# Kernel tuning notes

Measured on AMD Instinct MI355X. Metric: run time of the kernel, lower is better.

Reference implementation:

```python
import jax, jax.numpy as jnp
import numpy as np

EPS = 1e-5  # haiku LayerNorm default eps

def _ln(x):
    # LayerNorm over last dim, no scale/offset, use_fast_variance=False
    m = jnp.mean(x, axis=-1, keepdims=True)
    v = jnp.mean((x - m) ** 2, axis=-1, keepdims=True)
    return (x - m) / jnp.sqrt(v + EPS)

def _adaptive_ln(x, cond, gamma_c, Ws, bs, Wb):
    # AdaptiveLayerNorm with single_cond path
    xn = _ln(x)
    cn = _ln(cond) * gamma_c           # single_cond_layer_norm (scale only)
    scale = cn @ Ws + bs               # single_cond_scale (with bias)
    bias = cn @ Wb                     # single_cond_bias (no bias)
    return jax.nn.sigmoid(scale) * xn + bias

def setup_inputs() -> dict:
    key = jax.random.key(0)
    ks = jax.random.split(key, 24)
    B, Q, K, C, H = 2, 3072, 3072, 128, 4
    Dh = C // H
    s = 0.02
    inp = {
        'x_q': jax.random.normal(ks[0], (B, Q, C), jnp.float32),
        'x_k': jax.random.normal(ks[1], (B, K, C), jnp.float32),
        'mask_q': jax.random.randint(ks[2], (B, Q), 0, 2, jnp.int32),
        'mask_k': jax.random.randint(ks[3], (B, K), 0, 2, jnp.int32),
        'pair_logits': jax.random.normal(ks[4], (B, H, Q, K), jnp.float32),
        'single_cond_q': jax.random.normal(ks[5], (B, Q, C), jnp.float32),
        'single_cond_k': jax.random.normal(ks[6], (B, K, C), jnp.float32),
        # AdaptiveLayerNorm q params
        'gamma_cq': jnp.ones((C,), jnp.float32),
        'Wsq': jax.random.normal(ks[7], (C, C), jnp.float32) * s,
        'bsq': jax.random.normal(ks[8], (C,), jnp.float32) * s,
        'Wbq': jax.random.normal(ks[9], (C, C), jnp.float32) * s,
        # AdaptiveLayerNorm k params
        'gamma_ck': jnp.ones((C,), jnp.float32),
        'Wsk': jax.random.normal(ks[10], (C, C), jnp.float32) * s,
        'bsk': jax.random.normal(ks[11], (C,), jnp.float32) * s,
        'Wbk': jax.random.normal(ks[12], (C, C), jnp.float32) * s,
        # attention projections
        'Wq': jax.random.normal(ks[13], (C, H, Dh), jnp.float32) * s,
        'bq': jax.random.normal(ks[14], (1, H, Dh), jnp.float32) * s,
        'Wk': jax.random.normal(ks[15], (C, H, Dh), jnp.float32) * s,
        'Wv': jax.random.normal(ks[16], (C, H, Dh), jnp.float32) * s,
        'Wg': jax.random.normal(ks[17], (C, C), jnp.float32) * s,
        # AdaptiveZeroInit params
        'Wt2': jax.random.normal(ks[18], (C, C), jnp.float32) * s,
        'Wzc': jax.random.normal(ks[19], (C, C), jnp.float32) * s,
        'bzc': jax.random.normal(ks[20], (C,), jnp.float32) * s,
    }
    return inp

def reference(x_q, x_k, mask_q, mask_k, pair_logits, single_cond_q, single_cond_k,
              gamma_cq, Wsq, bsq, Wbq, gamma_ck, Wsk, bsk, Wbk,
              Wq, bq, Wk, Wv, Wg, Wt2, Wzc, bzc):
    mq = mask_q.astype(jnp.float32)
    mk = mask_k.astype(jnp.float32)
    # bias as written in the original: 1e9 * (mq-1)[...,None,:,None] * (mk-1)[...,None,None,:]
    bias = 1e9 * (mq - 1.0)[:, None, :, None] * (mk - 1.0)[:, None, None, :]
    bias = bias + pair_logits  # [B,H,Q,K]

    xq = _adaptive_ln(x_q, single_cond_q, gamma_cq, Wsq, bsq, Wbq)
    xk = _adaptive_ln(x_k, single_cond_k, gamma_ck, Wsk, bsk, Wbk)

    Dh = Wq.shape[-1]
    q = jnp.einsum('bqi,ihd->bqhd', xq, Wq) + bq  # bq [1,H,Dh] broadcasts
    k = jnp.einsum('bki,ihd->bkhd', xk, Wk)
    v = jnp.einsum('bki,ihd->bkhd', xk, Wv)

    logits = jnp.einsum('bqhd,bkhd->bhqk', q * (Dh ** -0.5), k) + bias
    weights = jax.nn.softmax(logits, axis=-1).astype(xq.dtype)
    wa = jnp.einsum('bhqk,bkhd->bqhd', weights, v)
    B, Q, H, _ = wa.shape
    wa = wa.reshape(B, Q, H * Dh)

    wa = wa * jax.nn.sigmoid(xq @ Wg)  # gating_query

    # AdaptiveZeroInit with raw single_cond_q
    out = (wa @ Wt2) * jax.nn.sigmoid(single_cond_q @ Wzc + bzc)
    return out
```

## Files before the change

kernel.cpp:

```cpp
#include <hip/hip_runtime.h>
#include <hip/hip_bf16.h>

typedef unsigned short u16;
typedef unsigned int u32;
typedef __attribute__((ext_vector_type(4))) float f32x4;
typedef __attribute__((ext_vector_type(4))) u32 u32x4;
typedef __attribute__((ext_vector_type(8))) __bf16 bf16x8;

#define SQ 3072
#define NH 4
#define DH 32

static __device__ __forceinline__ u16 f2bf(float f) {
  return __builtin_bit_cast(u16, (__bf16)f);
}
static __device__ __forceinline__ u32 pk2(float a, float b) {
  return (u32)f2bf(a) | ((u32)f2bf(b) << 16);
}
static __device__ __forceinline__ bf16x8 ld8(const u16* p) {
  return __builtin_bit_cast(bf16x8, *reinterpret_cast<const u32x4*>(p));
}
static __device__ __forceinline__ f32x4 mfma16(bf16x8 a, bf16x8 b, f32x4 c) {
  return __builtin_amdgcn_mfma_f32_16x16x32_bf16(a, b, c, 0, 0, 0);
}
static __device__ __forceinline__ float sigm(float x) { return 1.0f / (1.0f + __expf(-x)); }
static __device__ __forceinline__ float red16(float v) {
  v += __shfl_xor(v, 1); v += __shfl_xor(v, 2);
  v += __shfl_xor(v, 4); v += __shfl_xor(v, 8);
  return v;
}

static __device__ __forceinline__ void gemm8(
    const u16* a, const u16* wt, int lr, int lg, int w, f32x4 d[2]) {
  f32x4 z = {0.f, 0.f, 0.f, 0.f};
  d[0] = z; d[1] = z;
#pragma unroll
  for (int kc = 0; kc < 4; ++kc) {
    int ko = kc * 32 + lg * 8;
    bf16x8 a0 = ld8(a + lr * 136 + ko);
    bf16x8 a1 = ld8(a + (16 + lr) * 136 + ko);
    bf16x8 b0 = ld8(wt + (w * 16 + lr) * 128 + ko);
    d[0] = mfma16(a0, b0, d[0]);
    d[1] = mfma16(a1, b0, d[1]);
  }
}

struct PrepSrc { const float* p[10]; };

__global__ __launch_bounds__(256) void prep(PrepSrc s, u16* __restrict__ dst) {
  __shared__ float tl[32][132];
  const int mm = blockIdx.x >> 2, c = blockIdx.x & 3;
  const int tid = threadIdx.x;
  {
    const int krl = tid >> 3, col0 = (tid & 7) * 16;
    const int kr = c * 32 + krl;
    const float* src = s.p[mm] + kr * 128 + col0;
#pragma unroll
    for (int j = 0; j < 4; ++j) {
      f32x4 v = *reinterpret_cast<const f32x4*>(src + j * 4);
      tl[krl][col0 + j * 4 + 0] = v[0];
      tl[krl][col0 + j * 4 + 1] = v[1];
      tl[krl][col0 + j * 4 + 2] = v[2];
      tl[krl][col0 + j * 4 + 3] = v[3];
    }
  }
  __syncthreads();
  const int co = tid >> 1, kc0 = (tid & 1) * 16;
  u32 wbuf[8];
#pragma unroll
  for (int j = 0; j < 8; ++j)
    wbuf[j] = pk2(tl[kc0 + 2 * j][co], tl[kc0 + 2 * j + 1][co]);
  u32x4* dp = reinterpret_cast<u32x4*>(dst + mm * 16384 + co * 128 + c * 32 + kc0);
  u32x4 w0 = {wbuf[0], wbuf[1], wbuf[2], wbuf[3]};
  u32x4 w1 = {wbuf[4], wbuf[5], wbuf[6], wbuf[7]};
  dp[0] = w0; dp[1] = w1;
}

__global__ __launch_bounds__(512) void rowblocks(
    const float* __restrict__ x_q, const float* __restrict__ scq,
    const float* __restrict__ gamma_cq, const float* __restrict__ bsq,
    const float* __restrict__ bq, const float* __restrict__ bzc,
    const float* __restrict__ x_k, const float* __restrict__ sck,
    const float* __restrict__ gamma_ck, const float* __restrict__ bsk,
    const u16* __restrict__ WT,
    u16* __restrict__ qbf, float* __restrict__ gate, float* __restrict__ zc,
    u16* __restrict__ kbf, u16* __restrict__ vT) {
  __shared__ float xnf[32 * 132];
  __shared__ u16 a_cn[32 * 136];
  __shared__ u16 a_raw[32 * 136];
  __shared__ u16 a_xa[32 * 136];
  const int tid = threadIdx.x;
  const bool qside = blockIdx.x < 192;
  const int blk = qside ? blockIdx.x : blockIdx.x - 192;
  const float* x     = qside ? x_q : x_k;
  const float* cond  = qside ? scq : sck;
  const float* gamma = qside ? gamma_cq : gamma_ck;
  const float* bs    = qside ? bsq : bsk;
  const int rl = tid >> 4, sub = tid & 15, c0 = sub * 8;
  const size_t grow = (size_t)blk * 32 + rl;

  {
    float xs[8];
    const float4* xr = reinterpret_cast<const float4*>(x + grow * 128 + c0);
    float4 t0 = xr[0], t1 = xr[1];
    xs[0]=t0.x; xs[1]=t0.y; xs[2]=t0.z; xs[3]=t0.w;
    xs[4]=t1.x; xs[5]=t1.y; xs[6]=t1.z; xs[7]=t1.w;
    float s = 0.f;
#pragma unroll
    for (int i = 0; i < 8; ++i) s += xs[i];
    float mean = red16(s) * (1.f / 128.f);
    float vs = 0.f;
#pragma unroll
    for (int i = 0; i < 8; ++i) { float dd = xs[i] - mean; vs += dd * dd; }
    float rstd = rsqrtf(red16(vs) * (1.f / 128.f) + 1e-5f);
    float4* xw = reinterpret_cast<float4*>(&xnf[rl * 132 + c0]);
    float4 o0, o1;
    o0.x=(xs[0]-mean)*rstd; o0.y=(xs[1]-mean)*rstd; o0.z=(xs[2]-mean)*rstd; o0.w=(xs[3]-mean)*rstd;
    o1.x=(xs[4]-mean)*rstd; o1.y=(xs[5]-mean)*rstd; o1.z=(xs[6]-mean)*rstd; o1.w=(xs[7]-mean)*rstd;
    xw[0] = o0; xw[1] = o1;
  }
  {
    float cs[8], gs[8];
    const float4* cr = reinterpret_cast<const float4*>(cond + grow * 128 + c0);
    const float4* gr = reinterpret_cast<const float4*>(gamma + c0);
    float4 c_0 = cr[0], c_1 = cr[1], g_0 = gr[0], g_1 = gr[1];
    cs[0]=c_0.x; cs[1]=c_0.y; cs[2]=c_0.z; cs[3]=c_0.w;
    cs[4]=c_1.x; cs[5]=c_1.y; cs[6]=c_1.z; cs[7]=c_1.w;
    gs[0]=g_0.x; gs[1]=g_0.y; gs[2]=g_0.z; gs[3]=g_0.w;
    gs[4]=g_1.x; gs[5]=g_1.y; gs[6]=g_1.z; gs[7]=g_1.w;
    float s = 0.f;
#pragma unroll
    for (int i = 0; i < 8; ++i) s += cs[i];
    float mean = red16(s) * (1.f / 128.f);
    float vs = 0.f;
#pragma unroll
    for (int i = 0; i < 8; ++i) { float dd = cs[i] - mean; vs += dd * dd; }
    float rstd = rsqrtf(red16(vs) * (1.f / 128.f) + 1e-5f);
    float cn[8];
#pragma unroll
    for (int i = 0; i < 8; ++i) cn[i] = (cs[i] - mean) * rstd * gs[i];
    u32x4 cw = {pk2(cn[0],cn[1]), pk2(cn[2],cn[3]), pk2(cn[4],cn[5]), pk2(cn[6],cn[7])};
    *reinterpret_cast<u32x4*>(&a_cn[rl * 136 + c0]) = cw;
    if (qside) {
      u32x4 rw = {pk2(cs[0],cs[1]), pk2(cs[2],cs[3]), pk2(cs[4],cs[5]), pk2(cs[6],cs[7])};
      *reinterpret_cast<u32x4*>(&a_raw[rl * 136 + c0]) = rw;
    }
  }
  __syncthreads();
  const int lane = tid & 63, w = tid >> 6, lr = lane & 15, lg = lane >> 4;
  const int wtbase = qside ? 0 : 5;
  f32x4 dS[2], dB[2];
  gemm8(a_cn, WT + (wtbase + 0) * 16384, lr, lg, w, dS);
  gemm8(a_cn, WT + (wtbase + 1) * 16384, lr, lg, w, dB);
  const int col = w * 16 + lr;
#pragma unroll
  for (int mt = 0; mt < 2; ++mt)
#pragma unroll
    for (int r = 0; r < 4; ++r) {
      int rowl = mt * 16 + lg * 4 + r;
      float sc = dS[mt][r] + bs[col];
      float xa = sigm(sc) * xnf[rowl * 132 + col] + dB[mt][r];
      a_xa[rowl * 136 + col] = f2bf(xa);
    }
  __syncthreads();
  if (qside) {
    f32x4 dQ[2], dG[2], dZ[2];
    gemm8(a_xa,  WT + 2 * 16384, lr, lg, w, dQ);
    gemm8(a_xa,  WT + 3 * 16384, lr, lg, w, dG);
    gemm8(a_raw, WT + 4 * 16384, lr, lg, w, dZ);
#pragma unroll
    for (int mt = 0; mt < 2; ++mt)
#pragma unroll
      for (int r = 0; r < 4; ++r) {
        int rowl = mt * 16 + lg * 4 + r;
        size_t gr = (size_t)blk * 32 + rowl;
        int b = (int)(gr >= SQ);
        int pos = (int)gr - b * SQ;
        float qv = (dQ[mt][r] + bq[col]) * 0.17677669529663687f;
        qbf[(((size_t)b * NH + (col >> 5)) * SQ + pos) * DH + (col & 31)] = f2bf(qv);
        gate[gr * 128 + col] = sigm(dG[mt][r]);
        zc[gr * 128 + col] = sigm(dZ[mt][r] + bzc[col]);
      }
  } else {
    f32x4 dK[2], dV[2];
    gemm8(a_xa, WT + 7 * 16384, lr, lg, w, dK);
    gemm8(a_xa, WT + 8 * 16384, lr, lg, w, dV);
    const int h = col >> 5, dd = col & 31;
#pragma unroll
    for (int mt = 0; mt < 2; ++mt)
#pragma unroll
      for (int r = 0; r < 4; ++r) {
        int rowl = mt * 16 + lg * 4 + r;
        size_t gr = (size_t)blk * 32 + rowl;
        int b = (int)(gr >= SQ);
        int pos = (int)gr - b * SQ;
        kbf[(((size_t)b * NH + h) * SQ + pos) * DH + dd] = f2bf(dK[mt][r]);
        vT[(((size_t)b * NH + h) * DH + dd) * SQ + pos] = f2bf(dV[mt][r]);
      }
  }
}

__global__ __launch_bounds__(256) void attn(
    const u16* __restrict__ qbf, const u16* __restrict__ kbf, const u16* __restrict__ vT,
    const float* __restrict__ pair, const int* __restrict__ mask_q,
    const int* __restrict__ mask_k, const float* __restrict__ gate,
    u16* __restrict__ wa) {
  __shared__ float pbuf[2][16][260];
  __shared__ u16 plds[4][16 * 72];
  __shared__ float mb[4][16][34];
  const int tid = threadIdx.x, lane = tid & 63, w = tid >> 6, lr = lane & 15, lg = lane >> 4;
  const int bid = blockIdx.x;
  const int bh = bid & 7, qt = bid >> 3;
  const int b = bh >> 2, h = bh & 3;
  const int q0 = qt * 16;
  const bf16x8 aq = ld8(qbf + ((size_t)bh * SQ + q0 + lr) * DH + lg * 8);
  float mqm1[4];
#pragma unroll
  for (int r = 0; r < 4; ++r)
    mqm1[r] = 1e9f * ((float)mask_q[b * SQ + q0 + lg * 4 + r] - 1.f);
  float m[4], l[4];
#pragma unroll
  for (int r = 0; r < 4; ++r) { m[r] = -1e30f; l[r] = 0.f; }
  const f32x4 zero = {0.f, 0.f, 0.f, 0.f};
  f32x4 o[2]; o[0] = zero; o[1] = zero;
  const float* prow0 = pair + ((size_t)bh * SQ + q0 + w * 4) * SQ;
  u16* pw = plds[w];
  f32x4 pf[4];
#pragma unroll
  for (int j = 0; j < 4; ++j)
    pf[j] = __builtin_nontemporal_load(
        reinterpret_cast<const f32x4*>(prow0 + (size_t)j * SQ + lane * 4));
  for (int t = 0; t < 12; ++t) {
    const int bsel = t & 1;
#pragma unroll
    for (int j = 0; j < 4; ++j)
      *reinterpret_cast<f32x4*>(&pbuf[bsel][w * 4 + j][lane * 4]) = pf[j];
    __syncthreads();
    if (t < 11) {
#pragma unroll
      for (int j = 0; j < 4; ++j)
        pf[j] = __builtin_nontemporal_load(
            reinterpret_cast<const f32x4*>(prow0 + (size_t)j * SQ + (t + 1) * 256 + lane * 4));
    }
    const int kb = t * 256 + w * 64;
    f32x4 s[4];
#pragma unroll
    for (int kt = 0; kt < 4; ++kt)
      s[kt] = mfma16(aq, ld8(kbf + ((size_t)bh * SQ + kb + kt * 16 + lr) * DH + lg * 8), zero);
    float mk1[4];
#pragma unroll
    for (int kt = 0; kt < 4; ++kt)
      mk1[kt] = (float)mask_k[b * SQ + kb + kt * 16 + lr] - 1.f;
#pragma unroll
    for (int kt = 0; kt < 4; ++kt)
#pragma unroll
      for (int r = 0; r < 4; ++r) {
        float pv = pbuf[bsel][lg * 4 + r][w * 64 + kt * 16 + lr];
        s[kt][r] += fmaf(mqm1[r], mk1[kt], pv);
      }
    float alpha[4];
#pragma unroll
    for (int r = 0; r < 4; ++r) {
      float mx = fmaxf(fmaxf(s[0][r], s[1][r]), fmaxf(s[2][r], s[3][r]));
      mx = fmaxf(mx, __shfl_xor(mx, 1));
      mx = fmaxf(mx, __shfl_xor(mx, 2));
      mx = fmaxf(mx, __shfl_xor(mx, 4));
      mx = fmaxf(mx, __shfl_xor(mx, 8));
      float mn = fmaxf(m[r], mx);
      alpha[r] = __expf(m[r] - mn);
      m[r] = mn;
    }
#pragma unroll
    for (int r = 0; r < 4; ++r) {
      float acc = 0.f;
#pragma unroll
      for (int kt = 0; kt < 4; ++kt) {
        float p = __expf(s[kt][r] - m[r]);
        s[kt][r] = p;
        acc += p;
      }
      acc += __shfl_xor(acc, 1); acc += __shfl_xor(acc, 2);
      acc += __shfl_xor(acc, 4); acc += __shfl_xor(acc, 8);
      l[r] = l[r] * alpha[r] + acc;
      o[0][r] *= alpha[r];
      o[1][r] *= alpha[r];
    }
#pragma unroll
    for (int kt = 0; kt < 4; ++kt)
#pragma unroll
      for (int r = 0; r < 4; ++r)
        pw[(lg * 4 + r) * 72 + kt * 16 + lr] = f2bf(s[kt][r]);
#pragma unroll
    for (int kc = 0; kc < 2; ++kc) {
      bf16x8 pa = ld8(pw + lr * 72 + kc * 32 + lg * 8);
#pragma unroll
      for (int hf = 0; hf < 2; ++hf) {
        bf16x8 bv = ld8(vT + ((size_t)bh * DH + hf * 16 + lr) * SQ + kb + kc * 32 + lg * 8);
        o[hf] = mfma16(pa, bv, o[hf]);
      }
    }
  }
#pragma unroll
  for (int r = 0; r < 4; ++r) {
    int row = lg * 4 + r;
    mb[w][row][lr] = o[0][r];
    mb[w][row][16 + lr] = o[1][r];
    if (lr == 0) { mb[w][row][32] = m[r]; mb[w][row][33] = l[r]; }
  }
  __syncthreads();
#pragma unroll
  for (int it = 0; it < 2; ++it) {
    int q = (tid >> 5) + it * 8;
    int d = tid & 31;
    float m0 = mb[0][q][32], m1 = mb[1][q][32], m2 = mb[2][q][32], m3 = mb[3][q][32];
    float mm = fmaxf(fmaxf(m0, m1), fmaxf(m2, m3));
    float ll = 0.f, oo = 0.f;
#pragma unroll
    for (int w4 = 0; w4 < 4; ++w4) {
      float e = __expf(mb[w4][q][32] - mm);
      ll = fmaf(e, mb[w4][q][33], ll);
      oo = fmaf(e, mb[w4][q][d], oo);
    }
    size_t gi = ((size_t)b * SQ + q0 + q) * 128 + h * 32 + d;
    wa[gi] = f2bf((oo / ll) * gate[gi]);
  }
}

__global__ __launch_bounds__(512) void finalk(
    const u16* __restrict__ wa, const u16* __restrict__ WTt2,
    const float* __restrict__ zc, float* __restrict__ out) {
  __shared__ u16 awa[32 * 136];
  const int tid = threadIdx.x, rl = tid >> 4, sub = tid & 15, c0 = sub * 8;
  const size_t grow = (size_t)blockIdx.x * 32 + rl;
  *reinterpret_cast<u32x4*>(&awa[rl * 136 + c0]) =
      *reinterpret_cast<const u32x4*>(wa + grow * 128 + c0);
  __syncthreads();
  const int lane = tid & 63, w = tid >> 6, lr = lane & 15, lg = lane >> 4;
  f32x4 d[2];
  gemm8(awa, WTt2, lr, lg, w, d);
  const int col = w * 16 + lr;
#pragma unroll
  for (int mt = 0; mt < 2; ++mt)
#pragma unroll
    for (int r = 0; r < 4; ++r) {
      size_t gr = (size_t)blockIdx.x * 32 + mt * 16 + lg * 4 + r;
      out[gr * 128 + col] = d[mt][r] * zc[gr * 128 + col];
    }
}

extern "C" void kernel_launch(void* const* d_in, const int* in_sizes, int n_in,
                              void* d_out, int out_size, void* d_ws, size_t ws_size,
                              hipStream_t stream) {
  const float* x_q   = (const float*)d_in[0];
  const float* x_k   = (const float*)d_in[1];
  const int* mask_q  = (const int*)d_in[2];
  const int* mask_k  = (const int*)d_in[3];
  const float* pair  = (const float*)d_in[4];
  const float* scq   = (const float*)d_in[5];
  const float* sck   = (const float*)d_in[6];
  const float* gamma_cq = (const float*)d_in[7];
  const float* Wsq   = (const float*)d_in[8];
  const float* bsq   = (const float*)d_in[9];
  const float* Wbq   = (const float*)d_in[10];
  const float* gamma_ck = (const float*)d_in[11];
  const float* Wsk   = (const float*)d_in[12];
  const float* bsk   = (const float*)d_in[13];
  const float* Wbk   = (const float*)d_in[14];
  const float* Wq    = (const float*)d_in[15];
  const float* bq    = (const float*)d_in[16];
  const float* Wk    = (const float*)d_in[17];
  const float* Wv    = (const float*)d_in[18];
  const float* Wg    = (const float*)d_in[19];
  const float* Wt2   = (const float*)d_in[20];
  const float* Wzc   = (const float*)d_in[21];
  const float* bzc   = (const float*)d_in[22];

  char* wsb = (char*)d_ws;
  u16* WT     = (u16*)(wsb);
  u16* qbf    = (u16*)(wsb + 327680);
  u16* kbf    = (u16*)(wsb + 1900544);
  u16* vT     = (u16*)(wsb + 3473408);
  float* gate = (float*)(wsb + 5046272);
  float* zc   = (float*)(wsb + 8192000);
  u16* wa     = (u16*)(wsb + 11337728);
  float* out  = (float*)d_out;

  PrepSrc ps;
  ps.p[0] = Wsq; ps.p[1] = Wbq; ps.p[2] = Wq; ps.p[3] = Wg; ps.p[4] = Wzc;
  ps.p[5] = Wsk; ps.p[6] = Wbk; ps.p[7] = Wk; ps.p[8] = Wv; ps.p[9] = Wt2;

  hipLaunchKernelGGL(prep, dim3(40), dim3(256), 0, stream, ps, WT);
  hipLaunchKernelGGL(rowblocks, dim3(384), dim3(512), 0, stream,
                     x_q, scq, gamma_cq, bsq, bq, bzc,
                     x_k, sck, gamma_ck, bsk, WT, qbf, gate, zc, kbf, vT);
  hipLaunchKernelGGL(attn, dim3(8 * 192), dim3(256), 0, stream,
                     qbf, kbf, vT, pair, mask_q, mask_k, gate, wa);
  hipLaunchKernelGGL(finalk, dim3(192), dim3(512), 0, stream, wa, WT + 9 * 16384, zc, out);
}
```

Before: 120.2 us.

## Transpose QK MFMA, fold bias into accumulator, add lazy softmax rescale

The QK^T MFMA now runs with swapped operands, so each lane holds one query row across four keys. This replaces the 16-lane shuffle reductions with two cross-group shuffles per tile. The pair-logit and mask bias is loaded as a vector and passed in as the MFMA accumulator. Mask_k is precomputed as a float (mask-1) array in rowblocks, and the online-softmax rescale is skipped unless the running max grows by more than 8, with ds_bpermute redistributing alpha. P is written to LDS as packed bf16 pairs. The lazy rescale risks larger exponent ranges, and the extra mkf buffer adds a small write.

```diff
diff --git a/kernel.cpp b/kernel.cpp
--- a/kernel.cpp
+++ b/kernel.cpp
@@ -5,6 +5,7 @@
 typedef unsigned int u32;
 typedef __attribute__((ext_vector_type(4))) float f32x4;
 typedef __attribute__((ext_vector_type(4))) u32 u32x4;
+typedef __attribute__((ext_vector_type(2))) u32 u32x2;
 typedef __attribute__((ext_vector_type(8))) __bf16 bf16x8;
 
 #define SQ 3072
@@ -82,9 +83,9 @@
     const float* __restrict__ bq, const float* __restrict__ bzc,
     const float* __restrict__ x_k, const float* __restrict__ sck,
     const float* __restrict__ gamma_ck, const float* __restrict__ bsk,
-    const u16* __restrict__ WT,
+    const u16* __restrict__ WT, const int* __restrict__ mask_k,
     u16* __restrict__ qbf, float* __restrict__ gate, float* __restrict__ zc,
-    u16* __restrict__ kbf, u16* __restrict__ vT) {
+    u16* __restrict__ kbf, u16* __restrict__ vT, float* __restrict__ mkf) {
   __shared__ float xnf[32 * 132];
   __shared__ u16 a_cn[32 * 136];
   __shared__ u16 a_raw[32 * 136];
@@ -98,6 +99,10 @@
   const float* bs    = qside ? bsq : bsk;
   const int rl = tid >> 4, sub = tid & 15, c0 = sub * 8;
   const size_t grow = (size_t)blk * 32 + rl;
+  if (!qside && tid < 32) {
+    size_t g2 = (size_t)blk * 32 + tid;
+    mkf[g2] = (float)mask_k[g2] - 1.f;
+  }
 
   {
     float xs[8];
@@ -203,7 +208,7 @@
 __global__ __launch_bounds__(256) void attn(
     const u16* __restrict__ qbf, const u16* __restrict__ kbf, const u16* __restrict__ vT,
     const float* __restrict__ pair, const int* __restrict__ mask_q,
-    const int* __restrict__ mask_k, const float* __restrict__ gate,
+    const float* __restrict__ mkf, const float* __restrict__ gate,
     u16* __restrict__ wa) {
   __shared__ float pbuf[2][16][260];
   __shared__ u16 plds[4][16 * 72];
@@ -214,16 +219,12 @@
   const int b = bh >> 2, h = bh & 3;
   const int q0 = qt * 16;
   const bf16x8 aq = ld8(qbf + ((size_t)bh * SQ + q0 + lr) * DH + lg * 8);
-  float mqm1[4];
-#pragma unroll
-  for (int r = 0; r < 4; ++r)
-    mqm1[r] = 1e9f * ((float)mask_q[b * SQ + q0 + lg * 4 + r] - 1.f);
-  float m[4], l[4];
-#pragma unroll
-  for (int r = 0; r < 4; ++r) { m[r] = -1e30f; l[r] = 0.f; }
+  const float mqm1 = 1e9f * ((float)mask_q[b * SQ + q0 + lr] - 1.f);
+  float m = -1e30f, lsum = 0.f;
   const f32x4 zero = {0.f, 0.f, 0.f, 0.f};
   f32x4 o[2]; o[0] = zero; o[1] = zero;
   const float* prow0 = pair + ((size_t)bh * SQ + q0 + w * 4) * SQ;
+  const float* mrow = mkf + b * SQ;
   u16* pw = plds[w];
   f32x4 pf[4];
 #pragma unroll
@@ -245,51 +246,54 @@
     const int kb = t * 256 + w * 64;
     f32x4 s[4];
 #pragma unroll
+    for (int kt = 0; kt < 4; ++kt) {
+      bf16x8 kfv = ld8(kbf + ((size_t)bh * SQ + kb + kt * 16 + lr) * DH + lg * 8);
+      f32x4 pv = *reinterpret_cast<const f32x4*>(&pbuf[bsel][lr][w * 64 + kt * 16 + lg * 4]);
+      f32x4 mk = *reinterpret_cast<const f32x4*>(mrow + kb + kt * 16 + lg * 4);
+      f32x4 c;
+      c[0] = fmaf(mqm1, mk[0], pv[0]); c[1] = fmaf(mqm1, mk[1], pv[1]);
+      c[2] = fmaf(mqm1, mk[2], pv[2]); c[3] = fmaf(mqm1, mk[3], pv[3]);
+      s[kt] = mfma16(kfv, aq, c);
+    }
+    f32x4 mx = s[0];
+#pragma unroll
+    for (int kt = 1; kt < 4; ++kt)
+#pragma unroll
+      for (int r = 0; r < 4; ++r) mx[r] = fmaxf(mx[r], s[kt][r]);
+    float pm = fmaxf(fmaxf(mx[0], mx[1]), fmaxf(mx[2], mx[3]));
+    pm = fmaxf(pm, __shfl_xor(pm, 16));
+    pm = fmaxf(pm, __shfl_xor(pm, 32));
+    if (!__all(pm <= m + 8.f)) {
+      const float mn = fmaxf(m, pm);
+      const float alpha = __expf(m - mn);
+      m = mn;
+      float al[4];
+#pragma unroll
+      for (int r = 0; r < 4; ++r)
+        al[r] = __builtin_bit_cast(
+            float, __builtin_amdgcn_ds_bpermute((lg * 4 + r) << 2,
+                                                __builtin_bit_cast(int, alpha)));
+#pragma unroll
+      for (int hf = 0; hf < 2; ++hf)
+#pragma unroll
+        for (int r = 0; r < 4; ++r) o[hf][r] *= al[r];
+      lsum *= alpha;
+    }
+    float ps = 0.f;
+#pragma unroll
     for (int kt = 0; kt < 4; ++kt)
-      s[kt] = mfma16(aq, ld8(kbf + ((size_t)bh * SQ + kb + kt * 16 + lr) * DH + lg * 8), zero);
-    float mk1[4];
-#pragma unroll
-    for (int kt = 0; kt < 4; ++kt)
-      mk1[kt] = (float)mask_k[b * SQ + kb + kt * 16 + lr] - 1.f;
-#pragma unroll
-    for (int kt = 0; kt < 4; ++kt)
 #pragma unroll
       for (int r = 0; r < 4; ++r) {
-        float pv = pbuf[bsel][lg * 4 + r][w * 64 + kt * 16 + lr];
-        s[kt][r] += fmaf(mqm1[r], mk1[kt], pv);
+        float p = __expf(s[kt][r] - m);
+        s[kt][r] = p;
+        ps += p;
       }
-    float alpha[4];
-#pragma unroll
-    for (int r = 0; r < 4; ++r) {
-      float mx = fmaxf(fmaxf(s[0][r], s[1][r]), fmaxf(s[2][r], s[3][r]));
-      mx = fmaxf(mx, __shfl_xor(mx, 1));
-      mx = fmaxf(mx, __shfl_xor(mx, 2));
-      mx = fmaxf(mx, __shfl_xor(mx, 4));
-      mx = fmaxf(mx, __shfl_xor(mx, 8));
-      float mn = fmaxf(m[r], mx);
-      alpha[r] = __expf(m[r] - mn);
-      m[r] = mn;
-    }
-#pragma unroll
-    for (int r = 0; r < 4; ++r) {
-      float acc = 0.f;
-#pragma unroll
-      for (int kt = 0; kt < 4; ++kt) {
-        float p = __expf(s[kt][r] - m[r]);
-        s[kt][r] = p;
-        acc += p;
-      }
-      acc += __shfl_xor(acc, 1); acc += __shfl_xor(acc, 2);
-      acc += __shfl_xor(acc, 4); acc += __shfl_xor(acc, 8);
-      l[r] = l[r] * alpha[r] + acc;
-      o[0][r] *= alpha[r];
-      o[1][r] *= alpha[r];
-    }
-#pragma unroll
-    for (int kt = 0; kt < 4; ++kt)
-#pragma unroll
-      for (int r = 0; r < 4; ++r)
-        pw[(lg * 4 + r) * 72 + kt * 16 + lr] = f2bf(s[kt][r]);
+    lsum += ps;
+#pragma unroll
+    for (int kt = 0; kt < 4; ++kt) {
+      u32x2 pk = {pk2(s[kt][0], s[kt][1]), pk2(s[kt][2], s[kt][3])};
+      *reinterpret_cast<u32x2*>(pw + lr * 72 + kt * 16 + lg * 4) = pk;
+    }
 #pragma unroll
     for (int kc = 0; kc < 2; ++kc) {
       bf16x8 pa = ld8(pw + lr * 72 + kc * 32 + lg * 8);
@@ -300,13 +304,15 @@
       }
     }
   }
+  lsum += __shfl_xor(lsum, 16);
+  lsum += __shfl_xor(lsum, 32);
 #pragma unroll
   for (int r = 0; r < 4; ++r) {
     int row = lg * 4 + r;
     mb[w][row][lr] = o[0][r];
     mb[w][row][16 + lr] = o[1][r];
-    if (lr == 0) { mb[w][row][32] = m[r]; mb[w][row][33] = l[r]; }
-  }
+  }
+  if (lane < 16) { mb[w][lane][32] = m; mb[w][lane][33] = lsum; }
   __syncthreads();
 #pragma unroll
   for (int it = 0; it < 2; ++it) {
@@ -383,6 +389,7 @@
   float* gate = (float*)(wsb + 5046272);
   float* zc   = (float*)(wsb + 8192000);
   u16* wa     = (u16*)(wsb + 11337728);
+  float* mkf  = (float*)(wsb + 12910592);
   float* out  = (float*)d_out;
 
   PrepSrc ps;
@@ -392,8 +399,9 @@
   hipLaunchKernelGGL(prep, dim3(40), dim3(256), 0, stream, ps, WT);
   hipLaunchKernelGGL(rowblocks, dim3(384), dim3(512), 0, stream,
                      x_q, scq, gamma_cq, bsq, bq, bzc,
-                     x_k, sck, gamma_ck, bsk, WT, qbf, gate, zc, kbf, vT);
+                     x_k, sck, gamma_ck, bsk, WT, mask_k,
+                     qbf, gate, zc, kbf, vT, mkf);
   hipLaunchKernelGGL(attn, dim3(8 * 192), dim3(256), 0, stream,
-                     qbf, kbf, vT, pair, mask_q, mask_k, gate, wa);
+                     qbf, kbf, vT, pair, mask_q, mkf, gate, wa);
   hipLaunchKernelGGL(finalk, dim3(192), dim3(512), 0, stream, wa, WT + 9 * 16384, zc, out);
 }
```

After: 117.3 us. 2.4% less time.
